# Optimization experiments

Measured on AMD Instinct MI355X. Metric: run time of the kernel, lower is better.

The kernel has to match this reference:

```python
import jax, jax.numpy as jnp
import numpy as np

B, N, L, E = 4, 8, 2048, 16384
CH = [128, 256, 256, 256]
EPS = 1e-5
USE_MAX = True


def setup_inputs() -> dict:
    key = jax.random.key(0)
    ks = jax.random.split(key, 10)
    d = {}
    d["x"] = jax.random.normal(ks[0], (B, N, CH[0], L), jnp.float32)
    d["edge_index"] = jax.random.randint(ks[1], (2, E), 0, L, dtype=jnp.int32)
    wspecs = [("W1", CH[0], CH[1]), ("W2", CH[1], CH[2]), ("W3", CH[2], CH[3]),
              ("W1s", CH[0], CH[1]), ("W2s", CH[1], CH[2]), ("W3s", CH[2], CH[3])]
    for i, (nm, ci, co) in enumerate(wspecs):
        std = (2.0 / (ci + co)) ** 0.5  # xavier_normal
        d[nm] = std * jax.random.normal(ks[2 + i], (ci, co), jnp.float32)
        d["b" + nm[1:]] = jnp.zeros((co,), jnp.float32)
    for nm, co in [("1", CH[1]), ("2", CH[2]), ("3", CH[3]),
                   ("1s", CH[1]), ("2s", CH[2]), ("3s", CH[3])]:
        d["g" + nm] = jnp.ones((co,), jnp.float32)
        d["be" + nm] = jnp.zeros((co,), jnp.float32)
    return d


def _gcn_norm(edge_index, num_nodes):
    # PyG gcn_norm with improved=True: A_hat = A + 2I, sym normalization.
    src, dst = edge_index[0], edge_index[1]
    loop = jnp.arange(num_nodes, dtype=src.dtype)
    src = jnp.concatenate([src, loop])
    dst = jnp.concatenate([dst, loop])
    w = jnp.concatenate([jnp.ones((edge_index.shape[1],), jnp.float32),
                         jnp.full((num_nodes,), 2.0, jnp.float32)])
    deg = jnp.zeros((num_nodes,), jnp.float32).at[dst].add(w)
    dis = jnp.where(deg > 0, jax.lax.rsqrt(deg), 0.0)
    return src, dst, dis[src] * w * dis[dst]


def _gcn(h, W, bias, src, dst, norm, num_nodes):
    # h: [G, L, Cin] node features for G independent copies of the shared graph
    hw = h @ W  # [G, L, Cout]
    msgs = hw[:, src, :] * norm[None, :, None]  # gather along nodes
    agg = jnp.zeros((h.shape[0], num_nodes, W.shape[1]), h.dtype).at[:, dst].add(msgs)
    return agg + bias


def _bn(x, g, be):
    # x: [Nb, C, L]; training-mode BatchNorm1d over (Nb, L) per channel
    m = x.mean(axis=(0, 2), keepdims=True)
    v = x.var(axis=(0, 2), keepdims=True)
    return g[None, :, None] * (x - m) * jax.lax.rsqrt(v + EPS) + be[None, :, None]


def _forward(x, edge_index, params):
    b, n, c, l = x.shape
    src, dst, norm = _gcn_norm(edge_index, l)
    xo = None
    for (W, bias, Ws, bs, g, be, gs, bes) in params:
        # per-element branch
        h = x.reshape(b * n, x.shape[2], l).transpose(0, 2, 1)  # [b*n, L, C]
        x1 = _gcn(h, W, bias, src, dst, norm, l).transpose(0, 2, 1)  # [b*n, Cout, L]
        x1 = _bn(x1, g, be)
        # symmetric pooled branch
        xp = jnp.max(x, axis=1) if USE_MAX else jnp.sum(x, axis=1)  # [b, C, L]
        x2 = _gcn(xp.transpose(0, 2, 1), Ws, bs, src, dst, norm, l).transpose(0, 2, 1)
        x2 = _bn(x2, gs, bes)
        co = x2.shape[1]
        x2 = jnp.broadcast_to(x2[:, None], (b, n, co, l)).reshape(b * n, co, l)
        xo = jax.nn.relu(x1 + x2)  # [b*n, Cout, L]
        x = xo.reshape(b, n, co, l)
    return xo  # final output is [b*n, CH[3], L] (not reshaped back)


def reference(x, edge_index, W1, b1, W2, b2, W3, b3, W1s, b1s, W2s, b2s, W3s, b3s,
              g1, be1, g2, be2, g3, be3, g1s, be1s, g2s, be2s, g3s, be3s):
    params = [(W1, b1, W1s, b1s, g1, be1, g1s, be1s),
              (W2, b2, W2s, b2s, g2, be2, g2s, be2s),
              (W3, b3, W3s, b3s, g3, be3, g3s, be3s)]
    return _forward(x, edge_index, params)
```

## Files before the change

### kernel.cpp

```cpp
#include <hip/hip_runtime.h>
#include <math.h>

#define LNODES 2048
#define NEDGE 16384
#define GBIG 32
#define GSM 4
#define NCOUT 256
#define BN_EPS 1e-5f
#define ND 32

typedef unsigned short u16;
typedef __attribute__((ext_vector_type(8))) short bf16x8;
typedef __attribute__((ext_vector_type(4))) float f32x4;

__device__ __forceinline__ unsigned pk2(float a, float b) {
  unsigned ua = __float_as_uint(a); ua += 0x7fffu + ((ua >> 16) & 1u);
  unsigned ub = __float_as_uint(b); ub += 0x7fffu + ((ub >> 16) & 1u);
  return (ua >> 16) | (ub & 0xffff0000u);
}
__device__ __forceinline__ float blo(unsigned u) { return __uint_as_float(u << 16); }
__device__ __forceinline__ float bhi(unsigned u) { return __uint_as_float(u & 0xffff0000u); }

__device__ __forceinline__ void gl16(const u16* g, u16* l) {
  __builtin_amdgcn_global_load_lds(
      (const __attribute__((address_space(1))) void*)g,
      (__attribute__((address_space(3))) void*)l, 16, 0, 0);
}


__global__ __launch_bounds__(256) void count_deg_k(const int* __restrict__ ei,
                                                   float* __restrict__ deg,
                                                   int* __restrict__ cnt) {
  int e = blockIdx.x * 256 + threadIdx.x;
  if (e < NEDGE) {
    int d = ei[NEDGE + e];
    atomicAdd(&deg[d], 1.0f);
    atomicAdd(&cnt[d], 1);
  }
}

__global__ __launch_bounds__(256) void dis_k(const float* __restrict__ deg,
                                             float* __restrict__ dis,
                                             float* __restrict__ selfn) {
  int i = blockIdx.x * 256 + threadIdx.x;
  if (i < LNODES) {
    float di = rsqrtf(deg[i] + 2.0f);
    dis[i] = di;
    selfn[i] = 2.0f * di * di;
  }
}

__global__ __launch_bounds__(256) void scan_k(const int* __restrict__ cnt,
                                              int* __restrict__ rp) {
  __shared__ int part[256];
  int t = threadIdx.x;
  int base = t * 8;
  int loc[8];
  int s = 0;
#pragma unroll
  for (int j = 0; j < 8; ++j) { loc[j] = s; s += cnt[base + j]; }
  part[t] = s;
  __syncthreads();
  for (int off = 1; off < 256; off <<= 1) {
    int v = (t >= off) ? part[t - off] : 0;
    __syncthreads();
    part[t] += v;
    __syncthreads();
  }
  int excl = (t == 0) ? 0 : part[t - 1];
#pragma unroll
  for (int j = 0; j < 8; ++j) rp[base + j] = excl + loc[j];
  if (t == 255) rp[LNODES] = part[255];
}

__global__ __launch_bounds__(256) void fill_k(const int* __restrict__ ei,
                                              const int* __restrict__ rp,
                                              int* __restrict__ fillc,
                                              const float* __restrict__ dis,
                                              int* __restrict__ col,
                                              float* __restrict__ wn) {
  int e = blockIdx.x * 256 + threadIdx.x;
  if (e < NEDGE) {
    int s = ei[e], d = ei[NEDGE + e];
    int pos = rp[d] + atomicAdd(&fillc[d], 1);
    col[pos] = s;
    wn[pos] = dis[s] * dis[d];
  }
}

__global__ __launch_bounds__(256) void trans_k(const float* __restrict__ X,
                                               u16* __restrict__ XT, int Cin) {
  __shared__ float T[64][65];
  const int g = blockIdx.z;
  const int n0 = blockIdx.x * 64;
  const int c0 = blockIdx.y * 64;
  const int tr = threadIdx.x >> 4;
  const int tc = (threadIdx.x & 15) * 4;
#pragma unroll
  for (int p = 0; p < 4; ++p) {
    int ci = c0 + tr + p * 16;
    float4 v = *reinterpret_cast<const float4*>(&X[((size_t)g * Cin + ci) * LNODES + n0 + tc]);
    T[tr + p * 16][tc + 0] = v.x; T[tr + p * 16][tc + 1] = v.y;
    T[tr + p * 16][tc + 2] = v.z; T[tr + p * 16][tc + 3] = v.w;
  }
  __syncthreads();
#pragma unroll
  for (int p = 0; p < 4; ++p) {
    int nd = tr + p * 16;
    uint2 o = {pk2(T[tc + 0][nd], T[tc + 1][nd]), pk2(T[tc + 2][nd], T[tc + 3][nd])};
    *reinterpret_cast<uint2*>(&XT[((size_t)g * LNODES + n0 + nd) * Cin + c0 + tc]) = o;
  }
}

struct WCvt {
  const float* src[6];
  u16* dst[6];
  int ci[6];
};
__global__ __launch_bounds__(256) void cvtw_all_k(WCvt wp) {
  __shared__ float T[64][65];
  const int w = blockIdx.z;
  const int Ci = wp.ci[w];
  const int ci0 = blockIdx.y * 64;
  if (ci0 >= Ci) return;
  const float* W = wp.src[w];
  u16* WT = wp.dst[w];
  const int co0 = blockIdx.x * 64;
  const int tr = threadIdx.x >> 4;
  const int tc = (threadIdx.x & 15) * 4;
#pragma unroll
  for (int p = 0; p < 4; ++p) {
    int ci = ci0 + tr + p * 16;
    float4 v = *reinterpret_cast<const float4*>(&W[(size_t)ci * NCOUT + co0 + tc]);
    T[tr + p * 16][tc + 0] = v.x; T[tr + p * 16][tc + 1] = v.y;
    T[tr + p * 16][tc + 2] = v.z; T[tr + p * 16][tc + 3] = v.w;
  }
  __syncthreads();
  const int ci = ci0 + tc;
  const int kt = ci >> 5;
  const int kk = ci & 31;
#pragma unroll
  for (int p = 0; p < 4; ++p) {
    int co = co0 + tr + p * 16;
    uint2 o = {pk2(T[tc + 0][co - co0], T[tc + 1][co - co0]),
               pk2(T[tc + 2][co - co0], T[tc + 3][co - co0])};
    size_t idx = (size_t)kt * 8192 + (unsigned)((co * 32 + kk) ^ ((co & 7) << 3));
    *reinterpret_cast<uint2*>(&WT[idx]) = o;
  }
}

__global__ __launch_bounds__(256) void pool_bf_k(const u16* __restrict__ X,
                                                 u16* __restrict__ XP, int per) {
  int i = blockIdx.x * 256 + threadIdx.x;
  size_t f = (size_t)i * 8;
  int b = (int)(f / per);
  size_t rem = f - (size_t)b * per;
  const u16* base = X + (size_t)b * 8 * per + rem;
  uint4 u = *reinterpret_cast<const uint4*>(base);
  float m0 = blo(u.x), m1 = bhi(u.x), m2 = blo(u.y), m3 = bhi(u.y);
  float m4 = blo(u.z), m5 = bhi(u.z), m6 = blo(u.w), m7 = bhi(u.w);
#pragma unroll
  for (int j = 1; j < 8; ++j) {
    uint4 v = *reinterpret_cast<const uint4*>(base + (size_t)j * per);
    m0 = fmaxf(m0, blo(v.x)); m1 = fmaxf(m1, bhi(v.x));
    m2 = fmaxf(m2, blo(v.y)); m3 = fmaxf(m3, bhi(v.y));
    m4 = fmaxf(m4, blo(v.z)); m5 = fmaxf(m5, bhi(v.z));
    m6 = fmaxf(m6, blo(v.w)); m7 = fmaxf(m7, bhi(v.w));
  }
  uint4 o = {pk2(m0, m1), pk2(m2, m3), pk2(m4, m5), pk2(m6, m7)};
  *reinterpret_cast<uint4*>(XP + (size_t)b * per + rem) = o;
}

__device__ __forceinline__ void coef_ld(const float* __restrict__ st,
                                        const float* __restrict__ ga,
                                        const float* __restrict__ be,
                                        const float* __restrict__ gs,
                                        const float* __restrict__ bes,
                                        float* lk1, float* lk2, float* lcc, int t) {
  float sA = 0.f, qA = 0.f, sB = 0.f, qB = 0.f;
#pragma unroll
  for (int x = 0; x < 8; ++x) {
    sA += st[x * NCOUT + t];
    qA += st[2048 + x * NCOUT + t];
    sB += st[4096 + x * NCOUT + t];
    qB += st[6144 + x * NCOUT + t];
  }
  const float c1 = (float)(GBIG * LNODES), c2 = (float)(GSM * LNODES);
  float mA = sA / c1;
  float vA = qA / c1 - mA * mA;
  float kA = ga[t] * rsqrtf(vA + BN_EPS);
  float mB = sB / c2;
  float vB = qB / c2 - mB * mB;
  float kB = gs[t] * rsqrtf(vB + BN_EPS);
  lk1[t] = kA;
  lk2[t] = kB;
  lcc[t] = be[t] - kA * mA + bes[t] - kB * mB;
}

template <int MODE>
__global__ __launch_bounds__(256) void gemm3_k(const u16* __restrict__ B1,
                                               const u16* __restrict__ B2,
                                               const float* __restrict__ st,
                                               const float* __restrict__ ga,
                                               const float* __restrict__ be,
                                               const float* __restrict__ gs,
                                               const float* __restrict__ bes,
                                               const u16* __restrict__ WbT,
                                               const u16* __restrict__ WsT,
                                               u16* __restrict__ HW1,
                                               u16* __restrict__ hw2) {
  constexpr int Cin = (MODE == 0) ? 128 : 256;
  constexpr int BSH = 64 * Cin;
  constexpr int EPI = 64 * 264;
  constexpr int BASE = (BSH > EPI) ? BSH : EPI;
  __shared__ __align__(16) u16 smem[BASE + 8192];
  __shared__ float lk1[NCOUT], lk2[NCOUT], lcc[NCOUT];
  u16* Wsh = smem + BASE;
  const int z = blockIdx.z;
  const bool sym = z < GSM;
  const int g = sym ? z : z - GSM;
  u16* out = sym ? hw2 : HW1;
  const int n0 = blockIdx.x * 64;
  const int t = threadIdx.x;
  constexpr int OPR = Cin / 8;
  constexpr int RPI = 256 / OPR;
  constexpr int NIT = 64 / RPI;
  const int ro = t / OPR;
  const int ch8 = (t % OPR) * 8;

  float K1[8], K2[8], CC[8];
  if constexpr (MODE == 1) {
    coef_ld(st, ga, be, gs, bes, lk1, lk2, lcc, t);
    __syncthreads();
#pragma unroll
    for (int j = 0; j < 8; ++j) { K1[j] = lk1[ch8 + j]; K2[j] = lk2[ch8 + j]; CC[j] = lcc[ch8 + j]; }
  }

#define BIDX(r, c) ((((r) * Cin) + (c)) ^ (((r) & 7) << 3))

  if (MODE == 0 || sym) {
    if constexpr (MODE == 0) {
      const u16* src = (sym ? B2 : B1) + ((size_t)g * LNODES + n0) * Cin + ch8;
#pragma unroll
      for (int it = 0; it < NIT; ++it) {
        int row = it * RPI + ro;
        uint4 v = *reinterpret_cast<const uint4*>(&src[(size_t)row * Cin]);
        *reinterpret_cast<uint4*>(&smem[BIDX(row, ch8)]) = v;
      }
    } else {
      const size_t b2o = ((size_t)g * LNODES + n0) * NCOUT + ch8;
      const size_t a1b = ((size_t)(g * 8) * LNODES + n0) * NCOUT + ch8;
      const size_t nstep = (size_t)LNODES * NCOUT;
      for (int it = 0; it < NIT; ++it) {
        int row = it * RPI + ro;
        uint4 a2 = *reinterpret_cast<const uint4*>(&B2[b2o + (size_t)row * NCOUT]);
        float t0 = K2[0] * blo(a2.x) + CC[0], t1 = K2[1] * bhi(a2.x) + CC[1];
        float t2 = K2[2] * blo(a2.y) + CC[2], t3 = K2[3] * bhi(a2.y) + CC[3];
        float t4 = K2[4] * blo(a2.z) + CC[4], t5 = K2[5] * bhi(a2.z) + CC[5];
        float t6 = K2[6] * blo(a2.w) + CC[6], t7 = K2[7] * bhi(a2.w) + CC[7];
        float m0 = 0.f, m1 = 0.f, m2 = 0.f, m3 = 0.f, m4 = 0.f, m5 = 0.f, m6 = 0.f, m7 = 0.f;
#pragma unroll
        for (int n = 0; n < 8; ++n) {
          uint4 a1 = *reinterpret_cast<const uint4*>(&B1[a1b + n * nstep + (size_t)row * NCOUT]);
          m0 = fmaxf(m0, K1[0] * blo(a1.x) + t0); m1 = fmaxf(m1, K1[1] * bhi(a1.x) + t1);
          m2 = fmaxf(m2, K1[2] * blo(a1.y) + t2); m3 = fmaxf(m3, K1[3] * bhi(a1.y) + t3);
          m4 = fmaxf(m4, K1[4] * blo(a1.z) + t4); m5 = fmaxf(m5, K1[5] * bhi(a1.z) + t5);
          m6 = fmaxf(m6, K1[6] * blo(a1.w) + t6); m7 = fmaxf(m7, K1[7] * bhi(a1.w) + t7);
        }
        uint4 ov = {pk2(m0, m1), pk2(m2, m3), pk2(m4, m5), pk2(m6, m7)};
        *reinterpret_cast<uint4*>(&smem[BIDX(row, ch8)]) = ov;
      }
    }
  } else {
    const size_t b1o = ((size_t)g * LNODES + n0) * NCOUT + ch8;
    const size_t b2o = ((size_t)(g >> 3) * LNODES + n0) * NCOUT + ch8;
#pragma unroll
    for (int it = 0; it < NIT; ++it) {
      int row = it * RPI + ro;
      uint4 a1 = *reinterpret_cast<const uint4*>(&B1[b1o + (size_t)row * NCOUT]);
      uint4 a2 = *reinterpret_cast<const uint4*>(&B2[b2o + (size_t)row * NCOUT]);
      float o0 = fmaxf(K1[0] * blo(a1.x) + K2[0] * blo(a2.x) + CC[0], 0.f);
      float o1 = fmaxf(K1[1] * bhi(a1.x) + K2[1] * bhi(a2.x) + CC[1], 0.f);
      float o2 = fmaxf(K1[2] * blo(a1.y) + K2[2] * blo(a2.y) + CC[2], 0.f);
      float o3 = fmaxf(K1[3] * bhi(a1.y) + K2[3] * bhi(a2.y) + CC[3], 0.f);
      float o4 = fmaxf(K1[4] * blo(a1.z) + K2[4] * blo(a2.z) + CC[4], 0.f);
      float o5 = fmaxf(K1[5] * bhi(a1.z) + K2[5] * bhi(a2.z) + CC[5], 0.f);
      float o6 = fmaxf(K1[6] * blo(a1.w) + K2[6] * blo(a2.w) + CC[6], 0.f);
      float o7 = fmaxf(K1[7] * bhi(a1.w) + K2[7] * bhi(a2.w) + CC[7], 0.f);
      uint4 ov = {pk2(o0, o1), pk2(o2, o3), pk2(o4, o5), pk2(o6, o7)};
      *reinterpret_cast<uint4*>(&smem[BIDX(row, ch8)]) = ov;
    }
  }

  const int wv = t >> 6;
  const int lane = t & 63;
  const int q = lane >> 4, l = lane & 15;
  f32x4 zero = {0.f, 0.f, 0.f, 0.f};
  f32x4 acc[4][4];
#pragma unroll
  for (int i = 0; i < 4; ++i)
#pragma unroll
    for (int j = 0; j < 4; ++j) acc[i][j] = zero;

  const u16* Wmat = sym ? WsT : WbT;
#pragma unroll
  for (int kt = 0; kt < Cin / 32; ++kt) {
    __syncthreads();
    const u16* ws = Wmat + (size_t)kt * 8192;
#pragma unroll
    for (int c = 0; c < 4; ++c)
      gl16(ws + c * 2048 + t * 8, &Wsh[c * 2048 + t * 8]);
    __syncthreads();
    bf16x8 af[4], bx[4];
#pragma unroll
    for (int fi = 0; fi < 4; ++fi) {
      int row = wv * 64 + fi * 16 + l;
      af[fi] = *reinterpret_cast<const bf16x8*>(&Wsh[(row * 32 + q * 8) ^ ((row & 7) << 3)]);
    }
#pragma unroll
    for (int fj = 0; fj < 4; ++fj) {
      int brow = fj * 16 + l;
      bx[fj] = *reinterpret_cast<const bf16x8*>(&smem[BIDX(brow, kt * 32 + q * 8)]);
    }
#pragma unroll
    for (int fi = 0; fi < 4; ++fi)
#pragma unroll
      for (int fj = 0; fj < 4; ++fj)
        acc[fi][fj] = __builtin_amdgcn_mfma_f32_16x16x32_bf16(af[fi], bx[fj], acc[fi][fj], 0, 0, 0);
  }
#undef BIDX

  __syncthreads();
  u16* Csh = smem;
#pragma unroll
  for (int fi = 0; fi < 4; ++fi) {
#pragma unroll
    for (int fj = 0; fj < 4; ++fj) {
      int co_l = wv * 64 + fi * 16 + q * 4;
      int nd_l = fj * 16 + l;
      uint2 pkd = {pk2(acc[fi][fj][0], acc[fi][fj][1]),
                   pk2(acc[fi][fj][2], acc[fi][fj][3])};
      *reinterpret_cast<uint2*>(&Csh[nd_l * 264 + co_l]) = pkd;
    }
  }
  __syncthreads();
#pragma unroll
  for (int p = 0; p < 8; ++p) {
    int idx = p * 256 + t;
    int nd = idx >> 5;
    int c8 = (idx & 31) * 8;
    uint4 v = *reinterpret_cast<const uint4*>(&Csh[nd * 264 + c8]);
    *reinterpret_cast<uint4*>(&out[((size_t)g * LNODES + n0 + nd) * NCOUT + c8]) = v;
  }
}

__global__ __launch_bounds__(256) void agg_comb_k(const u16* __restrict__ HW1,
                                                  const u16* __restrict__ hw2,
                                                  const int* __restrict__ col,
                                                  const float* __restrict__ wn,
                                                  const int* __restrict__ rp,
                                                  const float* __restrict__ selfn,
                                                  u16* __restrict__ AGG1,
                                                  u16* __restrict__ agg2,
                                                  float* __restrict__ st) {
  __shared__ float lsum[8][NCOUT], lsq[8][NCOUT];
  const int bid = blockIdx.x;
  const int t = threadIdx.x;
  const int wv = t >> 6;
  float* sumO;
  float* sqO;
  int shard;
  if (bid < 1024) {
    int slot = bid >> 3;
    int chunk = slot & 63;
    int g0 = (bid & 7) + 8 * (slot >> 6);
    const int d0 = chunk * ND;
    const int h = (t >> 5) & 1;
    const int ch = (t & 31) * 8;
    const u16* baseh = HW1 + (size_t)(g0 + 16 * h) * LNODES * NCOUT;
    u16* outh = AGG1 + (size_t)(g0 + 16 * h) * LNODES * NCOUT;
    float s0 = 0.f, s1 = 0.f, s2 = 0.f, s3 = 0.f, s4 = 0.f, s5 = 0.f, s6 = 0.f, s7 = 0.f;
    float q0 = 0.f, q1 = 0.f, q2 = 0.f, q3 = 0.f, q4 = 0.f, q5 = 0.f, q6 = 0.f, q7 = 0.f;
    for (int i = wv; i < ND; i += 4) {
      int d = d0 + i;
      int e0 = rp[d], e1 = rp[d + 1];
      float sw = selfn[d];
      uint4 u = *reinterpret_cast<const uint4*>(&baseh[(size_t)d * NCOUT + ch]);
      float a0 = sw * blo(u.x), a1 = sw * bhi(u.x), a2 = sw * blo(u.y), a3 = sw * bhi(u.y);
      float a4 = sw * blo(u.z), a5 = sw * bhi(u.z), a6 = sw * blo(u.w), a7 = sw * bhi(u.w);
      int e = e0;
      const int e4 = e0 + ((e1 - e0) & ~3);
      for (; e < e4; e += 4) {
        int i0 = col[e + 0], i1 = col[e + 1], i2 = col[e + 2], i3 = col[e + 3];
        float w0 = wn[e + 0], w1 = wn[e + 1], w2 = wn[e + 2], w3 = wn[e + 3];
        uint4 v0 = *reinterpret_cast<const uint4*>(&baseh[(size_t)i0 * NCOUT + ch]);
        uint4 v1 = *reinterpret_cast<const uint4*>(&baseh[(size_t)i1 * NCOUT + ch]);
        uint4 v2 = *reinterpret_cast<const uint4*>(&baseh[(size_t)i2 * NCOUT + ch]);
        uint4 v3 = *reinterpret_cast<const uint4*>(&baseh[(size_t)i3 * NCOUT + ch]);
        a0 += w0 * blo(v0.x); a1 += w0 * bhi(v0.x); a2 += w0 * blo(v0.y); a3 += w0 * bhi(v0.y);
        a4 += w0 * blo(v0.z); a5 += w0 * bhi(v0.z); a6 += w0 * blo(v0.w); a7 += w0 * bhi(v0.w);
        a0 += w1 * blo(v1.x); a1 += w1 * bhi(v1.x); a2 += w1 * blo(v1.y); a3 += w1 * bhi(v1.y);
        a4 += w1 * blo(v1.z); a5 += w1 * bhi(v1.z); a6 += w1 * blo(v1.w); a7 += w1 * bhi(v1.w);
        a0 += w2 * blo(v2.x); a1 += w2 * bhi(v2.x); a2 += w2 * blo(v2.y); a3 += w2 * bhi(v2.y);
        a4 += w2 * blo(v2.z); a5 += w2 * bhi(v2.z); a6 += w2 * blo(v2.w); a7 += w2 * bhi(v2.w);
        a0 += w3 * blo(v3.x); a1 += w3 * bhi(v3.x); a2 += w3 * blo(v3.y); a3 += w3 * bhi(v3.y);
        a4 += w3 * blo(v3.z); a5 += w3 * bhi(v3.z); a6 += w3 * blo(v3.w); a7 += w3 * bhi(v3.w);
      }
      for (; e < e1; ++e) {
        int ci = col[e];
        float w = wn[e];
        uint4 v = *reinterpret_cast<const uint4*>(&baseh[(size_t)ci * NCOUT + ch]);
        a0 += w * blo(v.x); a1 += w * bhi(v.x); a2 += w * blo(v.y); a3 += w * bhi(v.y);
        a4 += w * blo(v.z); a5 += w * bhi(v.z); a6 += w * blo(v.w); a7 += w * bhi(v.w);
      }
      uint4 o = {pk2(a0, a1), pk2(a2, a3), pk2(a4, a5), pk2(a6, a7)};
      *reinterpret_cast<uint4*>(&outh[(size_t)d * NCOUT + ch]) = o;
      s0 += a0; s1 += a1; s2 += a2; s3 += a3; s4 += a4; s5 += a5; s6 += a6; s7 += a7;
      q0 += a0 * a0; q1 += a1 * a1; q2 += a2 * a2; q3 += a3 * a3;
      q4 += a4 * a4; q5 += a5 * a5; q6 += a6 * a6; q7 += a7 * a7;
    }
    int row = wv * 2 + h;
    float4 sa = {s0, s1, s2, s3}, sb = {s4, s5, s6, s7};
    float4 qa = {q0, q1, q2, q3}, qb = {q4, q5, q6, q7};
    *reinterpret_cast<float4*>(&lsum[row][ch]) = sa;
    *reinterpret_cast<float4*>(&lsum[row][ch + 4]) = sb;
    *reinterpret_cast<float4*>(&lsq[row][ch]) = qa;
    *reinterpret_cast<float4*>(&lsq[row][ch + 4]) = qb;
    sumO = st; sqO = st + 2048; shard = (bid & 7) * NCOUT;
  } else {
    int b2 = bid - 1024;
    int g = b2 & (GSM - 1);
    int chunk = b2 >> 2;
    const int d0 = chunk * ND;
    const int lc = (t & 63) * 4;
    const u16* base = hw2 + (size_t)g * LNODES * NCOUT;
    float4 s = {0.f, 0.f, 0.f, 0.f}, qq = {0.f, 0.f, 0.f, 0.f};
    for (int i = wv; i < ND; i += 4) {
      int d = d0 + i;
      int e0 = rp[d], e1 = rp[d + 1];
      float sw = selfn[d];
      uint2 u = *reinterpret_cast<const uint2*>(&base[(size_t)d * NCOUT + lc]);
      float4 a = {sw * blo(u.x), sw * bhi(u.x), sw * blo(u.y), sw * bhi(u.y)};
      int e = e0;
      const int e4 = e0 + ((e1 - e0) & ~3);
      for (; e < e4; e += 4) {
        int i0 = col[e + 0], i1 = col[e + 1], i2 = col[e + 2], i3 = col[e + 3];
        float w0 = wn[e + 0], w1 = wn[e + 1], w2 = wn[e + 2], w3 = wn[e + 3];
        uint2 v0 = *reinterpret_cast<const uint2*>(&base[(size_t)i0 * NCOUT + lc]);
        uint2 v1 = *reinterpret_cast<const uint2*>(&base[(size_t)i1 * NCOUT + lc]);
        uint2 v2 = *reinterpret_cast<const uint2*>(&base[(size_t)i2 * NCOUT + lc]);
        uint2 v3 = *reinterpret_cast<const uint2*>(&base[(size_t)i3 * NCOUT + lc]);
        a.x += w0 * blo(v0.x); a.y += w0 * bhi(v0.x); a.z += w0 * blo(v0.y); a.w += w0 * bhi(v0.y);
        a.x += w1 * blo(v1.x); a.y += w1 * bhi(v1.x); a.z += w1 * blo(v1.y); a.w += w1 * bhi(v1.y);
        a.x += w2 * blo(v2.x); a.y += w2 * bhi(v2.x); a.z += w2 * blo(v2.y); a.w += w2 * bhi(v2.y);
        a.x += w3 * blo(v3.x); a.y += w3 * bhi(v3.x); a.z += w3 * blo(v3.y); a.w += w3 * bhi(v3.y);
      }
      for (; e < e1; ++e) {
        float w = wn[e];
        uint2 v = *reinterpret_cast<const uint2*>(&base[(size_t)col[e] * NCOUT + lc]);
        a.x += w * blo(v.x); a.y += w * bhi(v.x); a.z += w * blo(v.y); a.w += w * bhi(v.y);
      }
      uint2 o = {pk2(a.x, a.y), pk2(a.z, a.w)};
      *reinterpret_cast<uint2*>(&agg2[((size_t)g * LNODES + d) * NCOUT + lc]) = o;
      s.x += a.x; s.y += a.y; s.z += a.z; s.w += a.w;
      qq.x += a.x * a.x; qq.y += a.y * a.y; qq.z += a.z * a.z; qq.w += a.w * a.w;
    }
    *reinterpret_cast<float4*>(&lsum[wv][lc]) = s;
    *reinterpret_cast<float4*>(&lsq[wv][lc]) = qq;
    float4 z4 = {0.f, 0.f, 0.f, 0.f};
    *reinterpret_cast<float4*>(&lsum[wv + 4][lc]) = z4;
    *reinterpret_cast<float4*>(&lsq[wv + 4][lc]) = z4;
    sumO = st + 4096; sqO = st + 6144; shard = (b2 & 7) * NCOUT;
  }
  __syncthreads();
  float ts = 0.f, tq = 0.f;
#pragma unroll
  for (int r = 0; r < 8; ++r) {
    ts += lsum[r][t];
    tq += lsq[r][t];
  }
  atomicAdd(&sumO[shard + t], ts);
  atomicAdd(&sqO[shard + t], tq);
}

__global__ __launch_bounds__(256) void fuse_tr_bf_k(const u16* __restrict__ A1,
                                                    const u16* __restrict__ A2,
                                                    const float* __restrict__ st,
                                                    const float* __restrict__ ga,
                                                    const float* __restrict__ be,
                                                    const float* __restrict__ gs,
                                                    const float* __restrict__ bes,
                                                    float* __restrict__ O) {
  __shared__ float T[64][65];
  __shared__ float lk1[NCOUT], lk2[NCOUT], lcc[NCOUT];
  const int g = blockIdx.z;
  const int d0 = blockIdx.x * 64;
  const int c0 = blockIdx.y * 64;
  const int b = g >> 3;
  const int t = threadIdx.x;
  coef_ld(st, ga, be, gs, bes, lk1, lk2, lcc, t);
  __syncthreads();
  const int tr = t >> 4;
  const int tc = (t & 15) * 4;
#pragma unroll
  for (int p = 0; p < 4; ++p) {
    int d = d0 + tr + p * 16;
    uint2 a1 = *reinterpret_cast<const uint2*>(&A1[((size_t)g * LNODES + d) * NCOUT + c0 + tc]);
    uint2 a2 = *reinterpret_cast<const uint2*>(&A2[((size_t)b * LNODES + d) * NCOUT + c0 + tc]);
    int cb = c0 + tc;
    T[tr + p * 16][tc + 0] = fmaxf(lk1[cb+0] * blo(a1.x) + lk2[cb+0] * blo(a2.x) + lcc[cb+0], 0.f);
    T[tr + p * 16][tc + 1] = fmaxf(lk1[cb+1] * bhi(a1.x) + lk2[cb+1] * bhi(a2.x) + lcc[cb+1], 0.f);
    T[tr + p * 16][tc + 2] = fmaxf(lk1[cb+2] * blo(a1.y) + lk2[cb+2] * blo(a2.y) + lcc[cb+2], 0.f);
    T[tr + p * 16][tc + 3] = fmaxf(lk1[cb+3] * bhi(a1.y) + lk2[cb+3] * bhi(a2.y) + lcc[cb+3], 0.f);
  }
  __syncthreads();
#pragma unroll
  for (int p = 0; p < 4; ++p) {
    int c = tr + p * 16;
    float4 o = {T[tc + 0][c], T[tc + 1][c], T[tc + 2][c], T[tc + 3][c]};
    *reinterpret_cast<float4*>(&O[((size_t)g * NCOUT + c0 + c) * LNODES + d0 + tc]) = o;
  }
}


extern "C" void kernel_launch(void* const* d_in, const int* in_sizes, int n_in,
                              void* d_out, int out_size, void* d_ws, size_t ws_size,
                              hipStream_t stream) {
  const float* x_in = (const float*)d_in[0];
  const int* ei = (const int*)d_in[1];
  const float* W[3]   = {(const float*)d_in[2],  (const float*)d_in[4],  (const float*)d_in[6]};
  const float* Wsym[3]= {(const float*)d_in[8],  (const float*)d_in[10], (const float*)d_in[12]};
  const float* ga[3]  = {(const float*)d_in[14], (const float*)d_in[16], (const float*)d_in[18]};
  const float* be[3]  = {(const float*)d_in[15], (const float*)d_in[17], (const float*)d_in[19]};
  const float* gs[3]  = {(const float*)d_in[20], (const float*)d_in[22], (const float*)d_in[24]};
  const float* bes[3] = {(const float*)d_in[21], (const float*)d_in[23], (const float*)d_in[25]};

  const size_t EBIG = (size_t)GBIG * LNODES * NCOUT;
  const size_t ESM = (size_t)GSM * LNODES * NCOUT;
  char* p = (char*)d_ws;
  u16* XT0  = (u16*)p; p += (size_t)GBIG * LNODES * 128 * 2;
  u16* AGG1 = (u16*)p; p += EBIG * 2;
  u16* agg2 = (u16*)p; p += ESM * 2;
  u16* xp   = (u16*)p; p += ESM * 2;
  u16* hw2  = (u16*)p; p += ESM * 2;
  u16* WbT[3], *WsT[3];
  for (int i = 0; i < 3; ++i) { WbT[i] = (u16*)p; p += NCOUT * NCOUT * 2; }
  for (int i = 0; i < 3; ++i) { WsT[i] = (u16*)p; p += NCOUT * NCOUT * 2; }
  int*   rp   = (int*)p;   p += 2064 * 4;
  float* dis  = (float*)p; p += LNODES * 4;
  float* selfn= (float*)p; p += LNODES * 4;
  char* zbase = p;
  float* deg  = (float*)p; p += LNODES * 4;
  int*   cnt  = (int*)p;   p += LNODES * 4;
  int*   fillc= (int*)p;   p += LNODES * 4;
  int*   col  = (int*)p;   p += (NEDGE + 8) * 4;
  float* wn   = (float*)p; p += (NEDGE + 8) * 4;
  float* stats= (float*)p; p += 3 * 4 * 2048 * 4;
  size_t zsize = (size_t)(p - zbase);

  u16* HW1 = (u16*)d_out;
  float* stL[3] = {stats, stats + 8192, stats + 16384};

  hipMemsetAsync(zbase, 0, zsize, stream);
  count_deg_k<<<NEDGE / 256, 256, 0, stream>>>(ei, deg, cnt);
  dis_k<<<LNODES / 256, 256, 0, stream>>>(deg, dis, selfn);
  scan_k<<<1, 256, 0, stream>>>(cnt, rp);
  fill_k<<<NEDGE / 256, 256, 0, stream>>>(ei, rp, fillc, dis, col, wn);
  WCvt wc;
  for (int i = 0; i < 3; ++i) {
    wc.src[i] = W[i];     wc.dst[i] = WbT[i];     wc.ci[i] = (i == 0) ? 128 : 256;
    wc.src[3 + i] = Wsym[i]; wc.dst[3 + i] = WsT[i]; wc.ci[3 + i] = (i == 0) ? 128 : 256;
  }
  cvtw_all_k<<<dim3(4, 4, 6), 256, 0, stream>>>(wc);
  trans_k<<<dim3(LNODES / 64, 128 / 64, GBIG), 256, 0, stream>>>(x_in, XT0, 128);
  pool_bf_k<<<GSM * 128 * LNODES / 8 / 256, 256, 0, stream>>>(XT0, xp, 128 * LNODES);

  dim3 ggrid(LNODES / 64, 1, GBIG + GSM);
  gemm3_k<0><<<ggrid, 256, 0, stream>>>(XT0, xp, nullptr, nullptr, nullptr, nullptr,
                                        nullptr, WbT[0], WsT[0], HW1, hw2);
  agg_comb_k<<<1280, 256, 0, stream>>>(HW1, hw2, col, wn, rp, selfn, AGG1, agg2, stL[0]);
  gemm3_k<1><<<ggrid, 256, 0, stream>>>(AGG1, agg2, stL[0], ga[0], be[0], gs[0], bes[0],
                                        WbT[1], WsT[1], HW1, hw2);
  agg_comb_k<<<1280, 256, 0, stream>>>(HW1, hw2, col, wn, rp, selfn, AGG1, agg2, stL[1]);
  gemm3_k<1><<<ggrid, 256, 0, stream>>>(AGG1, agg2, stL[1], ga[1], be[1], gs[1], bes[1],
                                        WbT[2], WsT[2], HW1, hw2);
  agg_comb_k<<<1280, 256, 0, stream>>>(HW1, hw2, col, wn, rp, selfn, AGG1, agg2, stL[2]);
  fuse_tr_bf_k<<<dim3(LNODES / 64, NCOUT / 64, GBIG), 256, 0, stream>>>(
      AGG1, agg2, stL[2], ga[2], be[2], gs[2], bes[2], (float*)d_out);
}
```

Measured before the change: 344.9 us.

## Merge setup kernels into three launches and register-prefetch GEMM weight tiles

Seven small setup kernels (degree count, weight conversion, input transpose, normalization, scan, CSR fill, max pooling) are merged into three launches. Each launch uses block-index ranges to run independent work side by side, which cuts launch overhead and serialization. In the GEMM, weight tiles are now prefetched into registers one k-step ahead and stored to LDS, replacing direct global-to-LDS loads, so the next tile's global latency overlaps the current MFMA work. This costs extra registers and may lower occupancy.

```diff
diff --git a/kernel.cpp b/kernel.cpp
--- a/kernel.cpp
+++ b/kernel.cpp
@@ -21,154 +21,151 @@
 __device__ __forceinline__ float blo(unsigned u) { return __uint_as_float(u << 16); }
 __device__ __forceinline__ float bhi(unsigned u) { return __uint_as_float(u & 0xffff0000u); }
 
-__device__ __forceinline__ void gl16(const u16* g, u16* l) {
-  __builtin_amdgcn_global_load_lds(
-      (const __attribute__((address_space(1))) void*)g,
-      (__attribute__((address_space(3))) void*)l, 16, 0, 0);
-}
-
-
-__global__ __launch_bounds__(256) void count_deg_k(const int* __restrict__ ei,
-                                                   float* __restrict__ deg,
-                                                   int* __restrict__ cnt) {
-  int e = blockIdx.x * 256 + threadIdx.x;
-  if (e < NEDGE) {
-    int d = ei[NEDGE + e];
-    atomicAdd(&deg[d], 1.0f);
-    atomicAdd(&cnt[d], 1);
-  }
-}
-
-__global__ __launch_bounds__(256) void dis_k(const float* __restrict__ deg,
-                                             float* __restrict__ dis,
-                                             float* __restrict__ selfn) {
-  int i = blockIdx.x * 256 + threadIdx.x;
-  if (i < LNODES) {
-    float di = rsqrtf(deg[i] + 2.0f);
-    dis[i] = di;
-    selfn[i] = 2.0f * di * di;
-  }
-}
-
-__global__ __launch_bounds__(256) void scan_k(const int* __restrict__ cnt,
-                                              int* __restrict__ rp) {
-  __shared__ int part[256];
-  int t = threadIdx.x;
-  int base = t * 8;
-  int loc[8];
-  int s = 0;
-#pragma unroll
-  for (int j = 0; j < 8; ++j) { loc[j] = s; s += cnt[base + j]; }
-  part[t] = s;
-  __syncthreads();
-  for (int off = 1; off < 256; off <<= 1) {
-    int v = (t >= off) ? part[t - off] : 0;
-    __syncthreads();
-    part[t] += v;
-    __syncthreads();
-  }
-  int excl = (t == 0) ? 0 : part[t - 1];
-#pragma unroll
-  for (int j = 0; j < 8; ++j) rp[base + j] = excl + loc[j];
-  if (t == 255) rp[LNODES] = part[255];
-}
-
-__global__ __launch_bounds__(256) void fill_k(const int* __restrict__ ei,
-                                              const int* __restrict__ rp,
-                                              int* __restrict__ fillc,
-                                              const float* __restrict__ dis,
-                                              int* __restrict__ col,
-                                              float* __restrict__ wn) {
-  int e = blockIdx.x * 256 + threadIdx.x;
-  if (e < NEDGE) {
-    int s = ei[e], d = ei[NEDGE + e];
-    int pos = rp[d] + atomicAdd(&fillc[d], 1);
-    col[pos] = s;
-    wn[pos] = dis[s] * dis[d];
-  }
-}
-
-__global__ __launch_bounds__(256) void trans_k(const float* __restrict__ X,
-                                               u16* __restrict__ XT, int Cin) {
-  __shared__ float T[64][65];
-  const int g = blockIdx.z;
-  const int n0 = blockIdx.x * 64;
-  const int c0 = blockIdx.y * 64;
-  const int tr = threadIdx.x >> 4;
-  const int tc = (threadIdx.x & 15) * 4;
-#pragma unroll
-  for (int p = 0; p < 4; ++p) {
-    int ci = c0 + tr + p * 16;
-    float4 v = *reinterpret_cast<const float4*>(&X[((size_t)g * Cin + ci) * LNODES + n0 + tc]);
-    T[tr + p * 16][tc + 0] = v.x; T[tr + p * 16][tc + 1] = v.y;
-    T[tr + p * 16][tc + 2] = v.z; T[tr + p * 16][tc + 3] = v.w;
-  }
-  __syncthreads();
-#pragma unroll
-  for (int p = 0; p < 4; ++p) {
-    int nd = tr + p * 16;
-    uint2 o = {pk2(T[tc + 0][nd], T[tc + 1][nd]), pk2(T[tc + 2][nd], T[tc + 3][nd])};
-    *reinterpret_cast<uint2*>(&XT[((size_t)g * LNODES + n0 + nd) * Cin + c0 + tc]) = o;
-  }
-}
 
 struct WCvt {
   const float* src[6];
   u16* dst[6];
   int ci[6];
 };
-__global__ __launch_bounds__(256) void cvtw_all_k(WCvt wp) {
+
+__global__ __launch_bounds__(256) void setup1_k(const int* __restrict__ ei,
+                                                float* __restrict__ deg,
+                                                int* __restrict__ cnt,
+                                                WCvt wp,
+                                                const float* __restrict__ x_in,
+                                                u16* __restrict__ XT0) {
   __shared__ float T[64][65];
-  const int w = blockIdx.z;
-  const int Ci = wp.ci[w];
-  const int ci0 = blockIdx.y * 64;
-  if (ci0 >= Ci) return;
-  const float* W = wp.src[w];
-  u16* WT = wp.dst[w];
-  const int co0 = blockIdx.x * 64;
-  const int tr = threadIdx.x >> 4;
-  const int tc = (threadIdx.x & 15) * 4;
-#pragma unroll
-  for (int p = 0; p < 4; ++p) {
-    int ci = ci0 + tr + p * 16;
-    float4 v = *reinterpret_cast<const float4*>(&W[(size_t)ci * NCOUT + co0 + tc]);
-    T[tr + p * 16][tc + 0] = v.x; T[tr + p * 16][tc + 1] = v.y;
-    T[tr + p * 16][tc + 2] = v.z; T[tr + p * 16][tc + 3] = v.w;
-  }
-  __syncthreads();
-  const int ci = ci0 + tc;
-  const int kt = ci >> 5;
-  const int kk = ci & 31;
-#pragma unroll
-  for (int p = 0; p < 4; ++p) {
-    int co = co0 + tr + p * 16;
-    uint2 o = {pk2(T[tc + 0][co - co0], T[tc + 1][co - co0]),
-               pk2(T[tc + 2][co - co0], T[tc + 3][co - co0])};
-    size_t idx = (size_t)kt * 8192 + (unsigned)((co * 32 + kk) ^ ((co & 7) << 3));
-    *reinterpret_cast<uint2*>(&WT[idx]) = o;
-  }
-}
-
-__global__ __launch_bounds__(256) void pool_bf_k(const u16* __restrict__ X,
-                                                 u16* __restrict__ XP, int per) {
-  int i = blockIdx.x * 256 + threadIdx.x;
-  size_t f = (size_t)i * 8;
-  int b = (int)(f / per);
-  size_t rem = f - (size_t)b * per;
-  const u16* base = X + (size_t)b * 8 * per + rem;
-  uint4 u = *reinterpret_cast<const uint4*>(base);
-  float m0 = blo(u.x), m1 = bhi(u.x), m2 = blo(u.y), m3 = bhi(u.y);
-  float m4 = blo(u.z), m5 = bhi(u.z), m6 = blo(u.w), m7 = bhi(u.w);
-#pragma unroll
-  for (int j = 1; j < 8; ++j) {
-    uint4 v = *reinterpret_cast<const uint4*>(base + (size_t)j * per);
-    m0 = fmaxf(m0, blo(v.x)); m1 = fmaxf(m1, bhi(v.x));
-    m2 = fmaxf(m2, blo(v.y)); m3 = fmaxf(m3, bhi(v.y));
-    m4 = fmaxf(m4, blo(v.z)); m5 = fmaxf(m5, bhi(v.z));
-    m6 = fmaxf(m6, blo(v.w)); m7 = fmaxf(m7, bhi(v.w));
-  }
-  uint4 o = {pk2(m0, m1), pk2(m2, m3), pk2(m4, m5), pk2(m6, m7)};
-  *reinterpret_cast<uint4*>(XP + (size_t)b * per + rem) = o;
+  const int bid = blockIdx.x;
+  const int t = threadIdx.x;
+  if (bid < 64) {
+    int e = bid * 256 + t;
+    int d = ei[NEDGE + e];
+    atomicAdd(&deg[d], 1.0f);
+    atomicAdd(&cnt[d], 1);
+  } else if (bid < 160) {
+    const int w = bid - 64;
+    const int bz = w >> 4;
+    const int Ci = wp.ci[bz];
+    const int ci0 = ((w >> 2) & 3) * 64;
+    if (ci0 >= Ci) return;
+    const float* W = wp.src[bz];
+    u16* WT = wp.dst[bz];
+    const int co0 = (w & 3) * 64;
+    const int tr = t >> 4;
+    const int tc = (t & 15) * 4;
+#pragma unroll
+    for (int p = 0; p < 4; ++p) {
+      int ci = ci0 + tr + p * 16;
+      float4 v = *reinterpret_cast<const float4*>(&W[(size_t)ci * NCOUT + co0 + tc]);
+      T[tr + p * 16][tc + 0] = v.x; T[tr + p * 16][tc + 1] = v.y;
+      T[tr + p * 16][tc + 2] = v.z; T[tr + p * 16][tc + 3] = v.w;
+    }
+    __syncthreads();
+    const int ci = ci0 + tc;
+    const int kt = ci >> 5;
+    const int kk = ci & 31;
+#pragma unroll
+    for (int p = 0; p < 4; ++p) {
+      int co = co0 + tr + p * 16;
+      uint2 o = {pk2(T[tc + 0][co - co0], T[tc + 1][co - co0]),
+                 pk2(T[tc + 2][co - co0], T[tc + 3][co - co0])};
+      size_t idx = (size_t)kt * 8192 + (unsigned)((co * 32 + kk) ^ ((co & 7) << 3));
+      *reinterpret_cast<uint2*>(&WT[idx]) = o;
+    }
+  } else {
+    const int w = bid - 160;
+    const int g = w >> 6;
+    const int n0 = (w & 31) * 64;
+    const int c0 = ((w >> 5) & 1) * 64;
+    const int tr = t >> 4;
+    const int tc = (t & 15) * 4;
+#pragma unroll
+    for (int p = 0; p < 4; ++p) {
+      int ci = c0 + tr + p * 16;
+      float4 v = *reinterpret_cast<const float4*>(&x_in[((size_t)g * 128 + ci) * LNODES + n0 + tc]);
+      T[tr + p * 16][tc + 0] = v.x; T[tr + p * 16][tc + 1] = v.y;
+      T[tr + p * 16][tc + 2] = v.z; T[tr + p * 16][tc + 3] = v.w;
+    }
+    __syncthreads();
+#pragma unroll
+    for (int p = 0; p < 4; ++p) {
+      int nd = tr + p * 16;
+      uint2 o = {pk2(T[tc + 0][nd], T[tc + 1][nd]), pk2(T[tc + 2][nd], T[tc + 3][nd])};
+      *reinterpret_cast<uint2*>(&XT0[((size_t)g * LNODES + n0 + nd) * 128 + c0 + tc]) = o;
+    }
+  }
+}
+
+__global__ __launch_bounds__(256) void setup2_k(const float* __restrict__ deg,
+                                                float* __restrict__ dis,
+                                                float* __restrict__ selfn,
+                                                const int* __restrict__ cnt,
+                                                int* __restrict__ rp) {
+  __shared__ int part[256];
+  const int t = threadIdx.x;
+  if (blockIdx.x == 8) {
+    int base = t * 8;
+    int loc[8];
+    int s = 0;
+#pragma unroll
+    for (int j = 0; j < 8; ++j) { loc[j] = s; s += cnt[base + j]; }
+    part[t] = s;
+    __syncthreads();
+    for (int off = 1; off < 256; off <<= 1) {
+      int v = (t >= off) ? part[t - off] : 0;
+      __syncthreads();
+      part[t] += v;
+      __syncthreads();
+    }
+    int excl = (t == 0) ? 0 : part[t - 1];
+#pragma unroll
+    for (int j = 0; j < 8; ++j) rp[base + j] = excl + loc[j];
+    if (t == 255) rp[LNODES] = part[255];
+  } else {
+    int i = blockIdx.x * 256 + t;
+    float di = rsqrtf(deg[i] + 2.0f);
+    dis[i] = di;
+    selfn[i] = 2.0f * di * di;
+  }
+}
+
+__global__ __launch_bounds__(256) void setup3_k(const int* __restrict__ ei,
+                                                const int* __restrict__ rp,
+                                                int* __restrict__ fillc,
+                                                const float* __restrict__ dis,
+                                                int* __restrict__ col,
+                                                float* __restrict__ wn,
+                                                const u16* __restrict__ X,
+                                                u16* __restrict__ XP) {
+  const int bid = blockIdx.x;
+  const int t = threadIdx.x;
+  if (bid < 64) {
+    int e = bid * 256 + t;
+    int s = ei[e], d = ei[NEDGE + e];
+    int pos = rp[d] + atomicAdd(&fillc[d], 1);
+    col[pos] = s;
+    wn[pos] = dis[s] * dis[d];
+  } else {
+    const int per = 128 * LNODES;
+    int i = (bid - 64) * 256 + t;
+    size_t f = (size_t)i * 8;
+    int b = (int)(f / per);
+    size_t rem = f - (size_t)b * per;
+    const u16* base = X + (size_t)b * 8 * per + rem;
+    uint4 u = *reinterpret_cast<const uint4*>(base);
+    float m0 = blo(u.x), m1 = bhi(u.x), m2 = blo(u.y), m3 = bhi(u.y);
+    float m4 = blo(u.z), m5 = bhi(u.z), m6 = blo(u.w), m7 = bhi(u.w);
+#pragma unroll
+    for (int j = 1; j < 8; ++j) {
+      uint4 v = *reinterpret_cast<const uint4*>(base + (size_t)j * per);
+      m0 = fmaxf(m0, blo(v.x)); m1 = fmaxf(m1, bhi(v.x));
+      m2 = fmaxf(m2, blo(v.y)); m3 = fmaxf(m3, bhi(v.y));
+      m4 = fmaxf(m4, blo(v.z)); m5 = fmaxf(m5, bhi(v.z));
+      m6 = fmaxf(m6, blo(v.w)); m7 = fmaxf(m7, bhi(v.w));
+    }
+    uint4 o = {pk2(m0, m1), pk2(m2, m3), pk2(m4, m5), pk2(m6, m7)};
+    *reinterpret_cast<uint4*>(XP + (size_t)b * per + rem) = o;
+  }
 }
 
 __device__ __forceinline__ void coef_ld(const float* __restrict__ st,
@@ -210,6 +207,7 @@
                                                u16* __restrict__ HW1,
                                                u16* __restrict__ hw2) {
   constexpr int Cin = (MODE == 0) ? 128 : 256;
+  constexpr int NT = Cin / 32;
   constexpr int BSH = 64 * Cin;
   constexpr int EPI = 64 * 264;
   constexpr int BASE = (BSH > EPI) ? BSH : EPI;
@@ -222,6 +220,13 @@
   u16* out = sym ? hw2 : HW1;
   const int n0 = blockIdx.x * 64;
   const int t = threadIdx.x;
+  const u16* Wmat = sym ? WsT : WbT;
+
+  uint4 wreg[4];
+#pragma unroll
+  for (int c = 0; c < 4; ++c)
+    wreg[c] = *reinterpret_cast<const uint4*>(Wmat + c * 2048 + t * 8);
+
   constexpr int OPR = Cin / 8;
   constexpr int RPI = 256 / OPR;
   constexpr int NIT = 64 / RPI;
@@ -302,14 +307,18 @@
 #pragma unroll
     for (int j = 0; j < 4; ++j) acc[i][j] = zero;
 
-  const u16* Wmat = sym ? WsT : WbT;
-#pragma unroll
-  for (int kt = 0; kt < Cin / 32; ++kt) {
+#pragma unroll
+  for (int kt = 0; kt < NT; ++kt) {
     __syncthreads();
-    const u16* ws = Wmat + (size_t)kt * 8192;
 #pragma unroll
     for (int c = 0; c < 4; ++c)
-      gl16(ws + c * 2048 + t * 8, &Wsh[c * 2048 + t * 8]);
+      *reinterpret_cast<uint4*>(&Wsh[c * 2048 + t * 8]) = wreg[c];
+    if (kt + 1 < NT) {
+      const u16* ws = Wmat + (size_t)(kt + 1) * 8192;
+#pragma unroll
+      for (int c = 0; c < 4; ++c)
+        wreg[c] = *reinterpret_cast<const uint4*>(ws + c * 2048 + t * 8);
+    }
     __syncthreads();
     bf16x8 af[4], bx[4];
 #pragma unroll
@@ -562,18 +571,14 @@
   float* stL[3] = {stats, stats + 8192, stats + 16384};
 
   hipMemsetAsync(zbase, 0, zsize, stream);
-  count_deg_k<<<NEDGE / 256, 256, 0, stream>>>(ei, deg, cnt);
-  dis_k<<<LNODES / 256, 256, 0, stream>>>(deg, dis, selfn);
-  scan_k<<<1, 256, 0, stream>>>(cnt, rp);
-  fill_k<<<NEDGE / 256, 256, 0, stream>>>(ei, rp, fillc, dis, col, wn);
   WCvt wc;
   for (int i = 0; i < 3; ++i) {
     wc.src[i] = W[i];     wc.dst[i] = WbT[i];     wc.ci[i] = (i == 0) ? 128 : 256;
     wc.src[3 + i] = Wsym[i]; wc.dst[3 + i] = WsT[i]; wc.ci[3 + i] = (i == 0) ? 128 : 256;
   }
-  cvtw_all_k<<<dim3(4, 4, 6), 256, 0, stream>>>(wc);
-  trans_k<<<dim3(LNODES / 64, 128 / 64, GBIG), 256, 0, stream>>>(x_in, XT0, 128);
-  pool_bf_k<<<GSM * 128 * LNODES / 8 / 256, 256, 0, stream>>>(XT0, xp, 128 * LNODES);
+  setup1_k<<<2208, 256, 0, stream>>>(ei, deg, cnt, wc, x_in, XT0);
+  setup2_k<<<9, 256, 0, stream>>>(deg, dis, selfn, cnt, rp);
+  setup3_k<<<576, 256, 0, stream>>>(ei, rp, fillc, dis, col, wn, XT0, xp);
 
   dim3 ggrid(LNODES / 64, 1, GBIG + GSM);
   gemm3_k<0><<<ggrid, 256, 0, stream>>>(XT0, xp, nullptr, nullptr, nullptr, nullptr,
```

Result: slower. 401.3 us (+16.4%).
